# Kernel tuning notes

Measured on AMD Instinct MI355X. Metric: run time of the kernel, lower is better.

The kernel has to match this reference:

```python
import jax, jax.numpy as jnp
import numpy as np

K = 3          # kernel size
STRIDE = 1
PAD = 1
DIL = 1


def setup_inputs() -> dict:
    key = jax.random.key(0)
    k1, k2, k3 = jax.random.split(key, 3)
    N, Cin, H, W = 8, 128, 64, 64
    Cout = 128
    x = jax.random.normal(k1, (N, Cin, H, W), dtype=jnp.float32)
    # offset channels: 2 * deformable_groups * K*K = 18, interleaved (dy, dx) per tap
    offset = jax.random.normal(k2, (N, 2 * K * K, H, W), dtype=jnp.float32)
    weight = jax.random.normal(k3, (Cout, Cin, K, K), dtype=jnp.float32) / np.sqrt(Cin * K * K)
    return {"x": x, "offset": offset, "weight": weight}


def _deform_conv(x, offset, weight):
    N, Cin, H, W = x.shape
    Cout = weight.shape[0]
    KK = K * K
    Ho, Wo = offset.shape[2], offset.shape[3]

    off = offset.reshape(N, KK, 2, Ho, Wo)
    dy = off[:, :, 0]  # [N, KK, Ho, Wo]
    dx = off[:, :, 1]

    kh = jnp.repeat(jnp.arange(K), K).astype(x.dtype)   # [KK]
    kw = jnp.tile(jnp.arange(K), K).astype(x.dtype)     # [KK]
    base_i = (jnp.arange(Ho) * STRIDE - PAD).astype(x.dtype)  # [Ho]
    base_j = (jnp.arange(Wo) * STRIDE - PAD).astype(x.dtype)  # [Wo]

    # Sampling positions: [N, KK, Ho, Wo]
    py = base_i[None, None, :, None] + (kh * DIL)[None, :, None, None] + dy
    px = base_j[None, None, None, :] + (kw * DIL)[None, :, None, None] + dx

    y0 = jnp.floor(py)
    x0 = jnp.floor(px)
    wy1 = py - y0
    wx1 = px - x0
    wy0 = 1.0 - wy1
    wx0 = 1.0 - wx1
    y0i = y0.astype(jnp.int32)
    x0i = x0.astype(jnp.int32)
    y1i = y0i + 1
    x1i = x0i + 1

    x_flat = x.reshape(N, Cin, H * W)

    def gather(yi, xi):
        # zero-padding outside the image
        mask = ((yi >= 0) & (yi < H) & (xi >= 0) & (xi < W)).astype(x.dtype)
        idx = jnp.clip(yi, 0, H - 1) * W + jnp.clip(xi, 0, W - 1)  # [N,KK,Ho,Wo]
        v = jnp.take_along_axis(x_flat, idx.reshape(N, 1, -1), axis=2)  # [N,Cin,KK*Ho*Wo]
        v = v.reshape(N, Cin, KK, Ho, Wo)
        return v * mask[:, None]

    sampled = (gather(y0i, x0i) * (wy0 * wx0)[:, None]
               + gather(y0i, x1i) * (wy0 * wx1)[:, None]
               + gather(y1i, x0i) * (wy1 * wx0)[:, None]
               + gather(y1i, x1i) * (wy1 * wx1)[:, None])  # [N,Cin,KK,Ho,Wo]

    w = weight.reshape(Cout, Cin, KK)
    return jnp.einsum('nckij,ock->noij', sampled, w)


def reference(x, offset, weight):
    return _deform_conv(x, offset, weight)
```

## Files before the change

### kernel.cpp

```cpp
#include <hip/hip_runtime.h>


#define H  64
#define W  64
#define CIN 128
#define COUT 128
#define NB 8
#define KK 9

typedef short bf16x8 __attribute__((ext_vector_type(8)));
typedef float f32x4  __attribute__((ext_vector_type(4)));

__device__ __forceinline__ unsigned short f2bf(float f) {
    unsigned u = __builtin_bit_cast(unsigned, f);
    u += 0x7FFFu + ((u >> 16) & 1u);
    return (unsigned short)(u >> 16);
}
__device__ __forceinline__ float lo_f(unsigned u) { return __builtin_bit_cast(float, u << 16); }
__device__ __forceinline__ float hi_f(unsigned u) { return __builtin_bit_cast(float, u & 0xFFFF0000u); }

__global__ void prep_all(const float* __restrict__ x, const float* __restrict__ w,
                         unsigned short* __restrict__ xt, unsigned short* __restrict__ wt) {
    int b = blockIdx.x;
    int t = threadIdx.x;
    if (b >= NB * H) {
        int idx = (b - NB * H) * 256 + t;
        if (idx < KK * COUT * CIN) {
            int kk = idx / (COUT * CIN);
            int r  = idx - kk * (COUT * CIN);
            int co = r >> 7;
            int c  = r & 127;
            wt[idx] = f2bf(w[(co * CIN + c) * KK + kk]);
        }
        return;
    }
    __shared__ float tile[CIN][W + 4];
    int n = b >> 6, y = b & 63;
    const float* src = x + ((size_t)n * CIN * H + y) * W;
    #pragma unroll
    for (int it = 0; it < 8; ++it) {
        int idx = it * 256 + t;
        int c  = idx >> 4;
        int x4 = (idx & 15) << 2;
        int xs = (x4 + ((c >> 5) << 4)) & 63;
        *(float4*)&tile[c][xs] = *(const float4*)(src + (size_t)c * H * W + x4);
    }
    __syncthreads();
    int xp = t >> 2;
    int cbch = (t & 3) << 5;
    int xr = (xp + ((cbch >> 5) << 4)) & 63;
    unsigned short* dst = xt + (((size_t)(n * H + y) * W + xp) * CIN + cbch);
    unsigned rr[16];
    #pragma unroll
    for (int i = 0; i < 16; ++i) {
        float v0 = tile[cbch + 2 * i][xr];
        float v1 = tile[cbch + 2 * i + 1][xr];
        rr[i] = (unsigned)f2bf(v0) | ((unsigned)f2bf(v1) << 16);
    }
    #pragma unroll
    for (int i = 0; i < 4; ++i)
        ((uint4*)dst)[i] = make_uint4(rr[4*i], rr[4*i+1], rr[4*i+2], rr[4*i+3]);
}

struct GatherCtx {
    const unsigned short *c00, *c01, *c10, *c11;
    float w00, w01, w10, w11;
};

__device__ __forceinline__ GatherCtx gather_setup(float dy, float dx, int ho, int wo, int kk,
                                                  const unsigned short* xbase) {
    GatherCtx g;
    float py = (float)(ho - 1 + kk / 3) + dy;
    float px = (float)(wo - 1 + kk % 3) + dx;
    float y0f = floorf(py), x0f = floorf(px);
    float wy1 = py - y0f, wx1 = px - x0f;
    float wy0 = 1.f - wy1, wx0 = 1.f - wx1;
    int y0 = (int)y0f, x0 = (int)x0f;
    int y1 = y0 + 1, x1 = x0 + 1;
    bool vy0 = (unsigned)y0 < (unsigned)H, vy1 = (unsigned)y1 < (unsigned)H;
    bool vx0 = (unsigned)x0 < (unsigned)W, vx1 = (unsigned)x1 < (unsigned)W;
    g.w00 = (vy0 && vx0) ? wy0 * wx0 : 0.f;
    g.w01 = (vy0 && vx1) ? wy0 * wx1 : 0.f;
    g.w10 = (vy1 && vx0) ? wy1 * wx0 : 0.f;
    g.w11 = (vy1 && vx1) ? wy1 * wx1 : 0.f;
    int yc0 = min(max(y0, 0), H - 1), yc1 = min(max(y1, 0), H - 1);
    int xc0 = min(max(x0, 0), W - 1), xc1 = min(max(x1, 0), W - 1);
    const unsigned short* r0 = xbase + (size_t)yc0 * W * CIN;
    const unsigned short* r1 = xbase + (size_t)yc1 * W * CIN;
    g.c00 = r0 + xc0 * CIN;  g.c01 = r0 + xc1 * CIN;
    g.c10 = r1 + xc0 * CIN;  g.c11 = r1 + xc1 * CIN;
    return g;
}

__device__ __forceinline__ void gather_issue(const GatherCtx& g, uint4* gv) {
    #pragma unroll
    for (int j = 0; j < 4; ++j) {
        gv[4*j+0] = *(const uint4*)(g.c00 + 8*j);
        gv[4*j+1] = *(const uint4*)(g.c01 + 8*j);
        gv[4*j+2] = *(const uint4*)(g.c10 + 8*j);
        gv[4*j+3] = *(const uint4*)(g.c11 + 8*j);
    }
}

__device__ __forceinline__ void gather_blend_store(const GatherCtx& g, const uint4* gv,
                                                   unsigned short* dst) {
    #pragma unroll
    for (int j = 0; j < 4; ++j) {
        const unsigned* a0 = (const unsigned*)&gv[4*j+0];
        const unsigned* a1 = (const unsigned*)&gv[4*j+1];
        const unsigned* a2 = (const unsigned*)&gv[4*j+2];
        const unsigned* a3 = (const unsigned*)&gv[4*j+3];
        unsigned rr[4];
        #pragma unroll
        for (int i = 0; i < 4; ++i) {
            float v0 = g.w00*lo_f(a0[i]) + g.w01*lo_f(a1[i]) + g.w10*lo_f(a2[i]) + g.w11*lo_f(a3[i]);
            float v1 = g.w00*hi_f(a0[i]) + g.w01*hi_f(a1[i]) + g.w10*hi_f(a2[i]) + g.w11*hi_f(a3[i]);
            rr[i] = (unsigned)f2bf(v0) | ((unsigned)f2bf(v1) << 16);
        }
        *(uint4*)(dst + 8*j) = make_uint4(rr[0], rr[1], rr[2], rr[3]);
    }
}

__global__ __launch_bounds__(512, 2) void deform_main(
        const float* __restrict__ offs, const unsigned short* __restrict__ xt,
        const unsigned short* __restrict__ wt, float* __restrict__ out) {
    __shared__ __attribute__((aligned(16))) unsigned short samp[2][128][CIN + 8];
    __shared__ __attribute__((aligned(16))) unsigned short wts [2][COUT][CIN + 8];

    int b = blockIdx.x;
    int n = b >> 5, ho2 = b & 31;
    int t = threadIdx.x;
    int lane = t & 63, wv = t >> 6;
    int lm = lane & 15, lq = lane >> 4;
    int rw = wv & 1;
    int cobase = (wv >> 1) << 5;
    int arow = (rw << 6) + lm;

    f32x4 acc[4][2];
    #pragma unroll
    for (int mt = 0; mt < 4; ++mt)
        #pragma unroll
        for (int nt = 0; nt < 2; ++nt) acc[mt][nt] = f32x4{0.f, 0.f, 0.f, 0.f};

    int p  = t >> 2;
    int cb = (t & 3) << 5;
    int ho = (ho2 << 1) + (p >> 6);
    int wo = p & 63;
    const float* offbase = offs + (size_t)n * 2 * KK * H * W + (size_t)ho * W + wo;
    const unsigned short* xbase = xt + (size_t)n * H * W * CIN + cb;
    unsigned short* sdst0 = &samp[0][p][cb];
    unsigned short* sdst1 = &samp[1][p][cb];

    int sco = t >> 2;
    int sch = (t & 3) << 5;
    const unsigned short* wsrc = wt + (size_t)sco * CIN + sch;
    unsigned short* wdst0 = &wts[0][sco][sch];
    unsigned short* wdst1 = &wts[1][sco][sch];

    float dyA, dxA;
    {
        float dy0 = offbase[0];
        float dx0 = offbase[(size_t)H * W];
        uint4 wg[4];
        #pragma unroll
        for (int i = 0; i < 4; ++i) wg[i] = *(const uint4*)(wsrc + (i << 3));
        GatherCtx g = gather_setup(dy0, dx0, ho, wo, 0, xbase);
        uint4 gv[16];
        gather_issue(g, gv);
        dyA = offbase[(size_t)(2) * H * W];
        dxA = offbase[(size_t)(3) * H * W];
        gather_blend_store(g, gv, sdst0);
        #pragma unroll
        for (int i = 0; i < 4; ++i) *(uint4*)(wdst0 + (i << 3)) = wg[i];
        __syncthreads();
    }

    for (int kk = 0; kk < KK; ++kk) {
        unsigned short (*sbuf)[CIN + 8] = samp[kk & 1];
        unsigned short (*wbuf)[CIN + 8] = wts[kk & 1];
        GatherCtx g;
        uint4 gv[16], wg[4];
        bool pre = (kk < KK - 1);
        if (pre) {
            g = gather_setup(dyA, dxA, ho, wo, kk + 1, xbase);
            gather_issue(g, gv);
            const unsigned short* wk = wsrc + ((size_t)(kk + 1) << 14);
            #pragma unroll
            for (int i = 0; i < 4; ++i) wg[i] = *(const uint4*)(wk + (i << 3));
            if (kk < KK - 2) {
                dyA = offbase[(size_t)(2 * (kk + 2)) * H * W];
                dxA = offbase[(size_t)(2 * (kk + 2) + 1) * H * W];
            }
        }
        __builtin_amdgcn_sched_barrier(0);

        #pragma unroll
        for (int ct = 0; ct < 4; ++ct) {
            bf16x8 a[4];
            #pragma unroll
            for (int mt = 0; mt < 4; ++mt)
                a[mt] = *(const bf16x8*)&sbuf[arow + (mt << 4)][(ct << 5) + (lq << 3)];
            bf16x8 bb[2];
            #pragma unroll
            for (int nt = 0; nt < 2; ++nt)
                bb[nt] = *(const bf16x8*)&wbuf[cobase + (nt << 4) + lm][(ct << 5) + (lq << 3)];
            #pragma unroll
            for (int mt = 0; mt < 4; ++mt)
                #pragma unroll
                for (int nt = 0; nt < 2; ++nt)
                    acc[mt][nt] = __builtin_amdgcn_mfma_f32_16x16x32_bf16(a[mt], bb[nt], acc[mt][nt], 0, 0, 0);
        }

        if (pre) {
            unsigned short* sd = (kk & 1) ? sdst0 : sdst1;
            unsigned short* wd = (kk & 1) ? wdst0 : wdst1;
            gather_blend_store(g, gv, sd);
            #pragma unroll
            for (int i = 0; i < 4; ++i) *(uint4*)(wd + (i << 3)) = wg[i];
        }
        __syncthreads();
    }

    int hoo = (ho2 << 1) + rw;
    #pragma unroll
    for (int mt = 0; mt < 4; ++mt) {
        int wob = (mt << 4) + (lq << 2);
        #pragma unroll
        for (int nt = 0; nt < 2; ++nt) {
            int co = cobase + (nt << 4) + lm;
            *(f32x4*)(out + (((size_t)(n * COUT + co) * H + hoo) * W + wob)) = acc[mt][nt];
        }
    }
}

extern "C" void kernel_launch(void* const* d_in, const int* in_sizes, int n_in,
                              void* d_out, int out_size, void* d_ws, size_t ws_size,
                              hipStream_t stream) {
    const float* x      = (const float*)d_in[0];
    const float* offset = (const float*)d_in[1];
    const float* weight = (const float*)d_in[2];
    float* out = (float*)d_out;

    unsigned short* xt = (unsigned short*)d_ws;
    unsigned short* wt = (unsigned short*)((char*)d_ws + (size_t)NB*H*W*CIN*2);

    int wblocks = (KK * COUT * CIN + 255) / 256;
    hipLaunchKernelGGL(prep_all, dim3(NB * H + wblocks), dim3(256), 0, stream,
                       x, weight, xt, wt);
    hipLaunchKernelGGL(deform_main, dim3(NB * H / 2), dim3(512), 0, stream,
                       offset, xt, wt, out);
}
```

Before: 110.4 us.

## Shrink deform tile to one output row, load weights straight into registers

The main kernel now processes one output row per 256-thread block (512 blocks instead of 256). Weight fragments are loaded directly from global memory into registers with ping-pong buffers instead of being staged through shared memory. The KK loop is unrolled with explicit double-buffered sample tiles. Block indexing is interleaved across the batch for better L2 locality, and the software bf16 rounding is replaced by the hardware v_cvt_pk_bf16_f32 instruction. This cuts shared memory use and sync work and raises block count. In exchange it adds register pressure and more redundant global weight reads per block.

Measured after the change: 115.2 us. 4.4% more time.

```diff
diff --git a/kernel.cpp b/kernel.cpp
--- a/kernel.cpp
+++ b/kernel.cpp
@@ -7,6 +7,7 @@
 #define COUT 128
 #define NB 8
 #define KK 9
+#define SROW (CIN + 8)
 
 typedef short bf16x8 __attribute__((ext_vector_type(8)));
 typedef float f32x4  __attribute__((ext_vector_type(4)));
@@ -15,6 +16,11 @@
     unsigned u = __builtin_bit_cast(unsigned, f);
     u += 0x7FFFu + ((u >> 16) & 1u);
     return (unsigned short)(u >> 16);
+}
+__device__ __forceinline__ unsigned cvt_pk_bf16(float lo, float hi) {
+    unsigned r;
+    asm("v_cvt_pk_bf16_f32 %0, %1, %2" : "=v"(r) : "v"(lo), "v"(hi));
+    return r;
 }
 __device__ __forceinline__ float lo_f(unsigned u) { return __builtin_bit_cast(float, u << 16); }
 __device__ __forceinline__ float hi_f(unsigned u) { return __builtin_bit_cast(float, u & 0xFFFF0000u); }
@@ -35,7 +41,7 @@
         return;
     }
     __shared__ float tile[CIN][W + 4];
-    int n = b >> 6, y = b & 63;
+    int n = b & 7, y = b >> 3;
     const float* src = x + ((size_t)n * CIN * H + y) * W;
     #pragma unroll
     for (int it = 0; it < 8; ++it) {
@@ -52,11 +58,8 @@
     unsigned short* dst = xt + (((size_t)(n * H + y) * W + xp) * CIN + cbch);
     unsigned rr[16];
     #pragma unroll
-    for (int i = 0; i < 16; ++i) {
-        float v0 = tile[cbch + 2 * i][xr];
-        float v1 = tile[cbch + 2 * i + 1][xr];
-        rr[i] = (unsigned)f2bf(v0) | ((unsigned)f2bf(v1) << 16);
-    }
+    for (int i = 0; i < 16; ++i)
+        rr[i] = cvt_pk_bf16(tile[cbch + 2 * i][xr], tile[cbch + 2 * i + 1][xr]);
     #pragma unroll
     for (int i = 0; i < 4; ++i)
         ((uint4*)dst)[i] = make_uint4(rr[4*i], rr[4*i+1], rr[4*i+2], rr[4*i+3]);
@@ -115,26 +118,61 @@
         for (int i = 0; i < 4; ++i) {
             float v0 = g.w00*lo_f(a0[i]) + g.w01*lo_f(a1[i]) + g.w10*lo_f(a2[i]) + g.w11*lo_f(a3[i]);
             float v1 = g.w00*hi_f(a0[i]) + g.w01*hi_f(a1[i]) + g.w10*hi_f(a2[i]) + g.w11*hi_f(a3[i]);
-            rr[i] = (unsigned)f2bf(v0) | ((unsigned)f2bf(v1) << 16);
+            rr[i] = cvt_pk_bf16(v0, v1);
         }
         *(uint4*)(dst + 8*j) = make_uint4(rr[0], rr[1], rr[2], rr[3]);
     }
 }
 
-__global__ __launch_bounds__(512, 2) void deform_main(
+#define LOADB(dst, kkv) { \
+    const unsigned short* wk_ = wlane + ((size_t)(kkv) << 14);  \
+    _Pragma("unroll") \
+    for (int nt_ = 0; nt_ < 2; ++nt_) \
+        _Pragma("unroll") \
+        for (int ct_ = 0; ct_ < 4; ++ct_) \
+            dst[nt_][ct_] = *(const bf16x8*)(wk_ + (nt_ << 11) + (ct_ << 5)); }
+
+#define MFMA_PHASE(PAR, BREG) { \
+    _Pragma("unroll") \
+    for (int ct_ = 0; ct_ < 4; ++ct_) { \
+        bf16x8 a_[4]; \
+        _Pragma("unroll") \
+        for (int mt_ = 0; mt_ < 4; ++mt_) \
+            a_[mt_] = *(const bf16x8*)&samp[PAR][lm + (mt_ << 4)][(ct_ << 5) + (lq << 3)]; \
+        _Pragma("unroll") \
+        for (int mt_ = 0; mt_ < 4; ++mt_) { \
+            acc[mt_][0] = __builtin_amdgcn_mfma_f32_16x16x32_bf16(a_[mt_], BREG[0][ct_], acc[mt_][0], 0, 0, 0); \
+            acc[mt_][1] = __builtin_amdgcn_mfma_f32_16x16x32_bf16(a_[mt_], BREG[1][ct_], acc[mt_][1], 0, 0, 0); } } }
+
+#define ITER(kkv, PAR, BCUR, BNXT, LAST) { \
+    GatherCtx g_; uint4 gv_[16]; \
+    if (!(LAST)) { \
+        g_ = gather_setup(dyA, dxA, ho, p, (kkv) + 1, xbase); \
+        gather_issue(g_, gv_); \
+        LOADB(BNXT, (kkv) + 1); \
+        if ((kkv) < KK - 2) { \
+            dyA = offbase[(size_t)(2 * ((kkv) + 2)) * H * W]; \
+            dxA = offbase[(size_t)(2 * ((kkv) + 2) + 1) * H * W]; \
+        } \
+    } \
+    __builtin_amdgcn_sched_barrier(0);  \
+    MFMA_PHASE(PAR, BCUR); \
+    if (!(LAST)) { \
+        gather_blend_store(g_, gv_, &samp[1 - (PAR)][p][cb]); \
+        __syncthreads(); \
+    } }
+
+__global__ __launch_bounds__(256, 2) void deform_main(
         const float* __restrict__ offs, const unsigned short* __restrict__ xt,
         const unsigned short* __restrict__ wt, float* __restrict__ out) {
-    __shared__ __attribute__((aligned(16))) unsigned short samp[2][128][CIN + 8];
-    __shared__ __attribute__((aligned(16))) unsigned short wts [2][COUT][CIN + 8];
+    __shared__ __attribute__((aligned(16))) unsigned short samp[2][64][SROW];
 
     int b = blockIdx.x;
-    int n = b >> 5, ho2 = b & 31;
+    int n = b & 7, ho = b >> 3;
     int t = threadIdx.x;
     int lane = t & 63, wv = t >> 6;
     int lm = lane & 15, lq = lane >> 4;
-    int rw = wv & 1;
-    int cobase = (wv >> 1) << 5;
-    int arow = (rw << 6) + lm;
+    int cobase = wv << 5;
 
     f32x4 acc[4][2];
     #pragma unroll
@@ -144,91 +182,39 @@
 
     int p  = t >> 2;
     int cb = (t & 3) << 5;
-    int ho = (ho2 << 1) + (p >> 6);
-    int wo = p & 63;
-    const float* offbase = offs + (size_t)n * 2 * KK * H * W + (size_t)ho * W + wo;
+    const float* offbase = offs + (size_t)n * 2 * KK * H * W + (size_t)ho * W + p;
     const unsigned short* xbase = xt + (size_t)n * H * W * CIN + cb;
-    unsigned short* sdst0 = &samp[0][p][cb];
-    unsigned short* sdst1 = &samp[1][p][cb];
-
-    int sco = t >> 2;
-    int sch = (t & 3) << 5;
-    const unsigned short* wsrc = wt + (size_t)sco * CIN + sch;
-    unsigned short* wdst0 = &wts[0][sco][sch];
-    unsigned short* wdst1 = &wts[1][sco][sch];
-
-    float dyA, dxA;
+    const unsigned short* wlane = wt + (((size_t)(cobase + lm)) << 7) + (lq << 3);
+
+    bf16x8 bA[2][4], bB[2][4];
+
+    float dyA = offbase[0];
+    float dxA = offbase[(size_t)H * W];
     {
-        float dy0 = offbase[0];
-        float dx0 = offbase[(size_t)H * W];
-        uint4 wg[4];
-        #pragma unroll
-        for (int i = 0; i < 4; ++i) wg[i] = *(const uint4*)(wsrc + (i << 3));
-        GatherCtx g = gather_setup(dy0, dx0, ho, wo, 0, xbase);
+        GatherCtx g = gather_setup(dyA, dxA, ho, p, 0, xbase);
         uint4 gv[16];
         gather_issue(g, gv);
-        dyA = offbase[(size_t)(2) * H * W];
-        dxA = offbase[(size_t)(3) * H * W];
-        gather_blend_store(g, gv, sdst0);
-        #pragma unroll
-        for (int i = 0; i < 4; ++i) *(uint4*)(wdst0 + (i << 3)) = wg[i];
+        LOADB(bA, 0);
+        dyA = offbase[(size_t)2 * H * W];
+        dxA = offbase[(size_t)3 * H * W];
+        gather_blend_store(g, gv, &samp[0][p][cb]);
         __syncthreads();
     }
 
-    for (int kk = 0; kk < KK; ++kk) {
-        unsigned short (*sbuf)[CIN + 8] = samp[kk & 1];
-        unsigned short (*wbuf)[CIN + 8] = wts[kk & 1];
-        GatherCtx g;
-        uint4 gv[16], wg[4];
-        bool pre = (kk < KK - 1);
-        if (pre) {
-            g = gather_setup(dyA, dxA, ho, wo, kk + 1, xbase);
-            gather_issue(g, gv);
-            const unsigned short* wk = wsrc + ((size_t)(kk + 1) << 14);
-            #pragma unroll
-            for (int i = 0; i < 4; ++i) wg[i] = *(const uint4*)(wk + (i << 3));
-            if (kk < KK - 2) {
-                dyA = offbase[(size_t)(2 * (kk + 2)) * H * W];
-                dxA = offbase[(size_t)(2 * (kk + 2) + 1) * H * W];
-            }
-        }
-        __builtin_amdgcn_sched_barrier(0);
-
-        #pragma unroll
-        for (int ct = 0; ct < 4; ++ct) {
-            bf16x8 a[4];
-            #pragma unroll
-            for (int mt = 0; mt < 4; ++mt)
-                a[mt] = *(const bf16x8*)&sbuf[arow + (mt << 4)][(ct << 5) + (lq << 3)];
-            bf16x8 bb[2];
-            #pragma unroll
-            for (int nt = 0; nt < 2; ++nt)
-                bb[nt] = *(const bf16x8*)&wbuf[cobase + (nt << 4) + lm][(ct << 5) + (lq << 3)];
-            #pragma unroll
-            for (int mt = 0; mt < 4; ++mt)
-                #pragma unroll
-                for (int nt = 0; nt < 2; ++nt)
-                    acc[mt][nt] = __builtin_amdgcn_mfma_f32_16x16x32_bf16(a[mt], bb[nt], acc[mt][nt], 0, 0, 0);
-        }
-
-        if (pre) {
-            unsigned short* sd = (kk & 1) ? sdst0 : sdst1;
-            unsigned short* wd = (kk & 1) ? wdst0 : wdst1;
-            gather_blend_store(g, gv, sd);
-            #pragma unroll
-            for (int i = 0; i < 4; ++i) *(uint4*)(wd + (i << 3)) = wg[i];
-        }
-        __syncthreads();
-    }
-
-    int hoo = (ho2 << 1) + rw;
+    for (int k2 = 0; k2 < 4; ++k2) {
+        int kk = k2 << 1;
+        ITER(kk,     0, bA, bB, false);
+        ITER(kk + 1, 1, bB, bA, false);
+    }
+    ITER(8, 0, bA, bB, true);
+
     #pragma unroll
     for (int mt = 0; mt < 4; ++mt) {
         int wob = (mt << 4) + (lq << 2);
         #pragma unroll
         for (int nt = 0; nt < 2; ++nt) {
             int co = cobase + (nt << 4) + lm;
-            *(f32x4*)(out + (((size_t)(n * COUT + co) * H + hoo) * W + wob)) = acc[mt][nt];
+            *(f32x4*)(out + (((size_t)(n * COUT + co) * H + ho) * W + wob)) = acc[mt][nt];
         }
     }
 }
@@ -247,6 +233,6 @@
     int wblocks = (KK * COUT * CIN + 255) / 256;
     hipLaunchKernelGGL(prep_all, dim3(NB * H + wblocks), dim3(256), 0, stream,
                        x, weight, xt, wt);
-    hipLaunchKernelGGL(deform_main, dim3(NB * H / 2), dim3(512), 0, stream,
+    hipLaunchKernelGGL(deform_main, dim3(NB * H), dim3(256), 0, stream,
                        offset, xt, wt, out);
 }
```
